# Kernel optimization log

Hardware: AMD Instinct MI355X
Metric: run time of the kernel (lower is better)

## Reference

```python
import jax, jax.numpy as jnp
import numpy as np

NUM_HEADS = 12
LN_EPS = 1e-5


def _layernorm(x, w, b):
    m = jnp.mean(x, axis=-1, keepdims=True)
    v = jnp.mean(jnp.square(x - m), axis=-1, keepdims=True)
    return (x - m) * jax.lax.rsqrt(v + LN_EPS) * w + b


def setup_inputs() -> dict:
    key = jax.random.key(0)
    ks = jax.random.split(key, 6)
    B, N, C, H = 8, 1024, 768, 3072
    s = 0.02
    return {
        "x": jax.random.normal(ks[0], (B, N, C), jnp.float32),
        "ln1_w": jnp.ones((C,), jnp.float32),
        "ln1_b": jnp.zeros((C,), jnp.float32),
        "qkv_w": jax.random.normal(ks[1], (3 * C, C), jnp.float32) * s,
        "qkv_b": jnp.zeros((3 * C,), jnp.float32),
        "proj_w": jax.random.normal(ks[2], (C, C), jnp.float32) * s,
        "proj_b": jnp.zeros((C,), jnp.float32),
        "ln2_w": jnp.ones((C,), jnp.float32),
        "ln2_b": jnp.zeros((C,), jnp.float32),
        "fc1_w": jax.random.normal(ks[3], (H, C), jnp.float32) * s,
        "fc1_b": jnp.zeros((H,), jnp.float32),
        "fc2_w": jax.random.normal(ks[4], (C, H), jnp.float32) * s,
        "fc2_b": jnp.zeros((C,), jnp.float32),
    }


def reference(x, ln1_w, ln1_b, qkv_w, qkv_b, proj_w, proj_b,
              ln2_w, ln2_b, fc1_w, fc1_b, fc2_w, fc2_b):
    B, N, C = x.shape
    H = NUM_HEADS
    d = C // H
    scale = d ** (-0.5)

    # --- attention on norm1(x) (size=None path, dropout rates are 0) ---
    h = _layernorm(x, ln1_w, ln1_b)
    qkv = h @ qkv_w.T + qkv_b                      # [B,N,3C]
    qkv = qkv.reshape(B, N, 3, H, d).transpose(2, 0, 3, 1, 4)  # [3,B,H,N,d]
    q, k, v = qkv[0], qkv[1], qkv[2]
    attn = jnp.einsum('bhqd,bhkd->bhqk', q, k) * scale
    attn = jax.nn.softmax(attn, axis=-1)
    o = jnp.einsum('bhqk,bhkd->bhqd', attn, v)     # [B,H,N,d]
    o = o.transpose(0, 2, 1, 3).reshape(B, N, C)
    x_attn = o @ proj_w.T + proj_b

    # --- residual + MLP ---
    x = x + x_attn
    h2 = _layernorm(x, ln2_w, ln2_b)
    h2 = jax.nn.gelu(h2 @ fc1_w.T + fc1_b, approximate=False)
    x = x + (h2 @ fc2_w.T + fc2_b)
    return x
```

## Files before the change

### kernel.cpp

```cpp
#include <hip/hip_runtime.h>
#include <cmath>

typedef __bf16 bf16;
typedef __bf16 bf16x8 __attribute__((ext_vector_type(8)));
typedef __bf16 bf16x4 __attribute__((ext_vector_type(4)));
typedef float floatx4 __attribute__((ext_vector_type(4)));

#define MFMA16(A, B, C) __builtin_amdgcn_mfma_f32_16x16x32_bf16((A), (B), (C), 0, 0, 0)

#define GLDS16(g, l)                                                   \
  __builtin_amdgcn_global_load_lds(                                    \
      (const __attribute__((address_space(1))) void*)(g),              \
      (__attribute__((address_space(3))) void*)(l), 16, 0, 0)

__global__ __launch_bounds__(256) void pre_kernel(
    const float* __restrict__ x, const float* __restrict__ g,
    const float* __restrict__ be, bf16* __restrict__ h1,
    const float* __restrict__ s0, bf16* __restrict__ d0, int n0,
    const float* __restrict__ s1, bf16* __restrict__ d1, int n1,
    const float* __restrict__ s2, bf16* __restrict__ d2, int n2,
    const float* __restrict__ s3, bf16* __restrict__ d3, int n3) {
  int bid = blockIdx.x;
  int t = threadIdx.x;
  if (bid < 8192) {
    const float* xr = x + (size_t)bid * 768;
    float v0 = xr[t], v1 = xr[t + 256], v2 = xr[t + 512];
    float s = v0 + v1 + v2;
    float s2 = v0 * v0 + v1 * v1 + v2 * v2;
#pragma unroll
    for (int o = 1; o < 64; o <<= 1) {
      s += __shfl_xor(s, o, 64);
      s2 += __shfl_xor(s2, o, 64);
    }
    __shared__ float red[8];
    int w = t >> 6, lane = t & 63;
    if (lane == 0) { red[w] = s; red[4 + w] = s2; }
    __syncthreads();
    float ts = red[0] + red[1] + red[2] + red[3];
    float ts2 = red[4] + red[5] + red[6] + red[7];
    float mean = ts * (1.0f / 768.0f);
    float var = ts2 * (1.0f / 768.0f) - mean * mean;
    float rstd = rsqrtf(var + 1e-5f);
    bf16* orow = h1 + (size_t)bid * 768;
    orow[t]       = (bf16)((v0 - mean) * rstd * g[t]       + be[t]);
    orow[t + 256] = (bf16)((v1 - mean) * rstd * g[t + 256] + be[t + 256]);
    orow[t + 512] = (bf16)((v2 - mean) * rstd * g[t + 512] + be[t + 512]);
    return;
  }
  int i = (bid - 8192) * 256 + t;
  const float* s;
  bf16* d;
  if (i < n0) { s = s0 + (size_t)i * 4; d = d0 + (size_t)i * 4; }
  else if ((i -= n0) < n1) { s = s1 + (size_t)i * 4; d = d1 + (size_t)i * 4; }
  else if ((i -= n1) < n2) { s = s2 + (size_t)i * 4; d = d2 + (size_t)i * 4; }
  else if ((i -= n2) < n3) { s = s3 + (size_t)i * 4; d = d3 + (size_t)i * 4; }
  else return;
  bf16x4 v;
  v[0] = (bf16)s[0]; v[1] = (bf16)s[1]; v[2] = (bf16)s[2]; v[3] = (bf16)s[3];
  *(bf16x4*)d = v;
}

__global__ __launch_bounds__(256) void ln_kernel(const float* __restrict__ x,
                                                 const float* __restrict__ g,
                                                 const float* __restrict__ be,
                                                 bf16* __restrict__ out) {
  int row = blockIdx.x;
  int t = threadIdx.x;
  const float* xr = x + (size_t)row * 768;
  float v0 = xr[t], v1 = xr[t + 256], v2 = xr[t + 512];
  float s = v0 + v1 + v2;
  float s2 = v0 * v0 + v1 * v1 + v2 * v2;
#pragma unroll
  for (int o = 1; o < 64; o <<= 1) {
    s += __shfl_xor(s, o, 64);
    s2 += __shfl_xor(s2, o, 64);
  }
  __shared__ float red[8];
  int w = t >> 6, lane = t & 63;
  if (lane == 0) { red[w] = s; red[4 + w] = s2; }
  __syncthreads();
  float ts = red[0] + red[1] + red[2] + red[3];
  float ts2 = red[4] + red[5] + red[6] + red[7];
  float mean = ts * (1.0f / 768.0f);
  float var = ts2 * (1.0f / 768.0f) - mean * mean;
  float rstd = rsqrtf(var + 1e-5f);
  bf16* orow = out + (size_t)row * 768;
  orow[t]       = (bf16)((v0 - mean) * rstd * g[t]       + be[t]);
  orow[t + 256] = (bf16)((v1 - mean) * rstd * g[t + 256] + be[t + 256]);
  orow[t + 512] = (bf16)((v2 - mean) * rstd * g[t + 512] + be[t + 512]);
}

constexpr int EP_BF16 = 0;
constexpr int EP_RES_F32 = 1;
constexpr int EP_GELU_BF16 = 2;

template <int EP, int NJ>
__global__ __launch_bounds__(256, 3) void gemm_bt(
    const bf16* __restrict__ A, const bf16* __restrict__ Bw,
    const float* __restrict__ bias, const float* __restrict__ resid,
    void* __restrict__ outp, int M, int N, int K) {
  __shared__ alignas(16) bf16 Asl[128 * 64];
  __shared__ alignas(16) bf16 Bsl[NJ * 32 * 64];
  int tid = threadIdx.x;
  int lane = tid & 63, w = tid >> 6;
  int wm = w >> 1, wn = w & 1;
  int q16 = lane & 15, quad = lane >> 4;
  int fid = blockIdx.x + gridDim.x * blockIdx.y;
  int nb = gridDim.x;
  int s = fid >> 3;
  int m0 = ((fid & 7) * (gridDim.y >> 3) + s / nb) * 128;
  int n0 = (s % nb) * (NJ * 32);

  floatx4 acc[4][NJ];
#pragma unroll
  for (int i = 0; i < 4; i++)
#pragma unroll
    for (int j = 0; j < NJ; j++) acc[i][j] = (floatx4){0.f, 0.f, 0.f, 0.f};

  int rIn = lane >> 3;
  int cg = (lane & 7) ^ rIn;
  const bf16* ag[4];
  const bf16* bg[NJ];
#pragma unroll
  for (int q = 0; q < 4; q++)
    ag[q] = A + (size_t)(m0 + (w * 4 + q) * 8 + rIn) * K + cg * 8;
#pragma unroll
  for (int q = 0; q < NJ; q++)
    bg[q] = Bw + (size_t)(n0 + (w * NJ + q) * 8 + rIn) * K + cg * 8;
  bf16* la = &Asl[w * 2048];
  bf16* lb = &Bsl[w * NJ * 512];

  int msel = q16 & 7;
  int offA[2][4], offB[2][NJ];
#pragma unroll
  for (int ks = 0; ks < 2; ks++) {
#pragma unroll
    for (int i = 0; i < 4; i++)
      offA[ks][i] = (wm * 64 + i * 16 + q16) * 64 + (((ks * 4 + quad) ^ msel)) * 8;
#pragma unroll
    for (int j = 0; j < NJ; j++)
      offB[ks][j] = (wn * 16 * NJ + j * 16 + q16) * 64 + (((ks * 4 + quad) ^ msel)) * 8;
  }

  for (int k0 = 0; k0 < K; k0 += 64) {
    __syncthreads();
#pragma unroll
    for (int q = 0; q < 4; q++) {
      GLDS16(ag[q], la + q * 512);
      ag[q] += 64;
    }
#pragma unroll
    for (int q = 0; q < NJ; q++) {
      GLDS16(bg[q], lb + q * 512);
      bg[q] += 64;
    }
    __syncthreads();
#pragma unroll
    for (int ks = 0; ks < 2; ks++) {
      bf16x8 af[4], bfr[NJ];
#pragma unroll
      for (int i = 0; i < 4; i++) af[i] = *(const bf16x8*)&Asl[offA[ks][i]];
#pragma unroll
      for (int j = 0; j < NJ; j++) bfr[j] = *(const bf16x8*)&Bsl[offB[ks][j]];
#pragma unroll
      for (int i = 0; i < 4; i++)
#pragma unroll
        for (int j = 0; j < NJ; j++) acc[i][j] = MFMA16(af[i], bfr[j], acc[i][j]);
    }
  }

#pragma unroll
  for (int i = 0; i < 4; i++) {
#pragma unroll
    for (int j = 0; j < NJ; j++) {
#pragma unroll
      for (int r = 0; r < 4; r++) {
        int m = m0 + wm * 64 + i * 16 + quad * 4 + r;
        int n = n0 + wn * 16 * NJ + j * 16 + q16;
        size_t idx = (size_t)m * N + n;
        float v = acc[i][j][r] + bias[n];
        if constexpr (EP == EP_BF16) {
          ((bf16*)outp)[idx] = (bf16)v;
        } else if constexpr (EP == EP_RES_F32) {
          ((float*)outp)[idx] = v + resid[idx];
        } else {
          float u = v * (2.3022083f + 0.1029443f * v * v);
          float e = __builtin_amdgcn_exp2f(-u);
          float gv = v * __builtin_amdgcn_rcpf(1.0f + e);
          ((bf16*)outp)[idx] = (bf16)gv;
        }
      }
    }
  }
}

__global__ __launch_bounds__(256) void vt_kernel(const bf16* __restrict__ qkv,
                                                 bf16* __restrict__ VT) {
  __shared__ bf16 T[64 * 74];
  int t = threadIdx.x;
  int bh = blockIdx.y;
  int b = bh / 12, h = bh % 12;
  int kt = blockIdx.x;
  int kloc = t >> 2;
  int d0 = (t & 3) * 16;
  const bf16* src = qkv + (size_t)(b * 1024 + kt * 64 + kloc) * 2304 + 1536 +
                    h * 64 + d0;
  bf16x8 a = *(const bf16x8*)src;
  bf16x8 c = *(const bf16x8*)(src + 8);
#pragma unroll
  for (int e = 0; e < 8; e++) T[(d0 + e) * 74 + kloc] = a[e];
#pragma unroll
  for (int e = 0; e < 8; e++) T[(d0 + 8 + e) * 74 + kloc] = c[e];
  __syncthreads();
  int d = t >> 2;
  int k0 = (t & 3) * 16;
  bf16x8 r0, r1;
#pragma unroll
  for (int e = 0; e < 8; e++) r0[e] = T[d * 74 + k0 + e];
#pragma unroll
  for (int e = 0; e < 8; e++) r1[e] = T[d * 74 + k0 + 8 + e];
  bf16* dst = VT + ((size_t)bh * 64 + d) * 1024 + kt * 64 + k0;
  *(bf16x8*)dst = r0;
  *(bf16x8*)(dst + 8) = r1;
}

__global__ __launch_bounds__(256, 4) void attn_kernel(const bf16* __restrict__ qkv,
                                                      const bf16* __restrict__ VT,
                                                      bf16* __restrict__ o) {
  __shared__ alignas(16) bf16 Pl[4][2][16 * 40];
  int tid = threadIdx.x;
  int lane = tid & 63, w = tid >> 6;
  int q16 = lane & 15, quad = lane >> 4;
  int bh = blockIdx.y;
  int b = bh / 12, h = bh % 12;
  int qbase = blockIdx.x * 128 + w * 32;
  const int KS = 32 * 2304;

  bf16x8 qf[2][2];
#pragma unroll
  for (int qt = 0; qt < 2; qt++)
#pragma unroll
    for (int c = 0; c < 2; c++)
      qf[qt][c] = *(const bf16x8*)(qkv +
          (size_t)(b * 1024 + qbase + qt * 16 + q16) * 2304 + h * 64 +
          c * 32 + quad * 8);

  const bf16* kp[2];
#pragma unroll
  for (int nc = 0; nc < 2; nc++)
    kp[nc] = qkv + (size_t)(b * 1024 + nc * 16 + q16) * 2304 + 768 + h * 64 +
             quad * 8;
  const bf16* vp[4];
#pragma unroll
  for (int dc = 0; dc < 4; dc++)
    vp[dc] = VT + ((size_t)bh * 64 + dc * 16 + q16) * 1024 + quad * 8;

  const bf16* pread = &Pl[w][0][q16 * 40 + quad * 8];
  int pw_base = (quad * 4) * 40 + q16;

  float l_[2][4];
  floatx4 oacc[2][4];
#pragma unroll
  for (int qt = 0; qt < 2; qt++)
#pragma unroll
    for (int r = 0; r < 4; r++) l_[qt][r] = 0.f;
#pragma unroll
  for (int qt = 0; qt < 2; qt++)
#pragma unroll
    for (int dc = 0; dc < 4; dc++) oacc[qt][dc] = (floatx4){0.f, 0.f, 0.f, 0.f};

  for (int kt = 0; kt < 32; kt++) {
    bf16x8 kf[2][2];
#pragma unroll
    for (int nc = 0; nc < 2; nc++) {
#pragma unroll
      for (int ck = 0; ck < 2; ck++)
        kf[nc][ck] = *(const bf16x8*)(kp[nc] + ck * 32);
      kp[nc] += KS;
    }
    bf16x8 vf[4];
#pragma unroll
    for (int dc = 0; dc < 4; dc++) {
      vf[dc] = *(const bf16x8*)vp[dc];
      vp[dc] += 32;
    }

#pragma unroll
    for (int qt = 0; qt < 2; qt++) {
#pragma unroll
      for (int nc = 0; nc < 2; nc++) {
        floatx4 z = (floatx4){0.f, 0.f, 0.f, 0.f};
        z = MFMA16(qf[qt][0], kf[nc][0], z);
        z = MFMA16(qf[qt][1], kf[nc][1], z);
#pragma unroll
        for (int r = 0; r < 4; r++) {
          float p = __builtin_amdgcn_exp2f(z[r] * 0.18033688011f);
          l_[qt][r] += p;
          Pl[w][qt][pw_base + r * 40 + nc * 16] = (bf16)p;
        }
      }
    }

#pragma unroll
    for (int qt = 0; qt < 2; qt++) {
      bf16x8 pf = *(const bf16x8*)(pread + qt * 640);
#pragma unroll
      for (int dc = 0; dc < 4; dc++)
        oacc[qt][dc] = MFMA16(pf, vf[dc], oacc[qt][dc]);
    }
  }

#pragma unroll
  for (int qt = 0; qt < 2; qt++) {
    bf16* op = o + (size_t)(b * 1024 + qbase + qt * 16) * 768 + h * 64;
#pragma unroll
    for (int r = 0; r < 4; r++) {
      float s = l_[qt][r];
#pragma unroll
      for (int off = 1; off < 16; off <<= 1) s += __shfl_xor(s, off, 16);
      float inv = 1.0f / s;
#pragma unroll
      for (int dc = 0; dc < 4; dc++)
        op[(size_t)(quad * 4 + r) * 768 + dc * 16 + q16] =
            (bf16)(oacc[qt][dc][r] * inv);
    }
  }
}

extern "C" void kernel_launch(void* const* d_in, const int* in_sizes, int n_in,
                              void* d_out, int out_size, void* d_ws, size_t ws_size,
                              hipStream_t stream) {
  (void)in_sizes; (void)n_in; (void)out_size; (void)ws_size;
  const float* x      = (const float*)d_in[0];
  const float* ln1_w  = (const float*)d_in[1];
  const float* ln1_b  = (const float*)d_in[2];
  const float* qkv_w  = (const float*)d_in[3];
  const float* qkv_b  = (const float*)d_in[4];
  const float* proj_w = (const float*)d_in[5];
  const float* proj_b = (const float*)d_in[6];
  const float* ln2_w  = (const float*)d_in[7];
  const float* ln2_b  = (const float*)d_in[8];
  const float* fc1_w  = (const float*)d_in[9];
  const float* fc1_b  = (const float*)d_in[10];
  const float* fc2_w  = (const float*)d_in[11];
  const float* fc2_b  = (const float*)d_in[12];

  char* ws = (char*)d_ws;
  size_t off = 0;
  auto alloc = [&](size_t bytes) {
    void* p = ws + off;
    off += (bytes + 255) & ~(size_t)255;
    return p;
  };
  bf16* wq  = (bf16*)alloc((size_t)2304 * 768 * 2);
  bf16* wp  = (bf16*)alloc((size_t)768 * 768 * 2);
  bf16* wf1 = (bf16*)alloc((size_t)3072 * 768 * 2);
  bf16* wf2 = (bf16*)alloc((size_t)768 * 3072 * 2);
  bf16* slotA = (bf16*)alloc((size_t)8192 * 768 * 2);
  bf16* slotB = (bf16*)alloc((size_t)8192 * 3072 * 2);
  float* x1 = (float*)alloc((size_t)8192 * 768 * 4);
  bf16* VT = (bf16*)alloc((size_t)96 * 64 * 1024 * 2);

  bf16* h1 = slotA;
  bf16* qkvb = slotB;
  bf16* ob = slotA;
  bf16* h2 = slotA;
  bf16* hm = slotB;

  pre_kernel<<<8192 + 6912, 256, 0, stream>>>(
      x, ln1_w, ln1_b, h1,
      qkv_w, wq, 2304 * 768 / 4, proj_w, wp, 768 * 768 / 4,
      fc1_w, wf1, 3072 * 768 / 4, fc2_w, wf2, 768 * 3072 / 4);

  gemm_bt<EP_BF16, 4><<<dim3(18, 64), 256, 0, stream>>>(
      h1, wq, qkv_b, nullptr, qkvb, 8192, 2304, 768);
  vt_kernel<<<dim3(16, 96), 256, 0, stream>>>(qkvb, VT);
  attn_kernel<<<dim3(8, 96), 256, 0, stream>>>(qkvb, VT, ob);
  gemm_bt<EP_RES_F32, 2><<<dim3(12, 64), 256, 0, stream>>>(
      ob, wp, proj_b, x, x1, 8192, 768, 768);
  ln_kernel<<<8192, 256, 0, stream>>>(x1, ln2_w, ln2_b, h2);
  gemm_bt<EP_GELU_BF16, 4><<<dim3(24, 64), 256, 0, stream>>>(
      h2, wf1, fc1_b, nullptr, hm, 8192, 3072, 768);
  gemm_bt<EP_RES_F32, 2><<<dim3(12, 64), 256, 0, stream>>>(
      hm, wf2, fc2_b, x1, (float*)d_out, 8192, 768, 3072);
}
```

Baseline: 367.0 us.

## Stage K/V tiles in LDS with async double buffering and transpose S

The attention kernel now loads each 32-key K and V tile once per block into swizzled LDS through global_load_lds, double buffered so the next tile's load overlaps the current tile's compute. It no longer has every wave read K and V straight from global memory. S is computed transposed (K as the A operand), so the softmax probabilities land directly in registers in the layout the 16x16x16 MFMA needs. This removes the per-tile LDS round trip for P. Block indexing is flattened so that consecutive blocks map to different batches, which changes L2 locality. The cost is a block-wide barrier every iteration and twice as many smaller MFMAs for P·V.

```diff
diff --git a/kernel.cpp b/kernel.cpp
--- a/kernel.cpp
+++ b/kernel.cpp
@@ -5,8 +5,14 @@
 typedef __bf16 bf16x8 __attribute__((ext_vector_type(8)));
 typedef __bf16 bf16x4 __attribute__((ext_vector_type(4)));
 typedef float floatx4 __attribute__((ext_vector_type(4)));
+typedef short short4v __attribute__((ext_vector_type(4)));
 
 #define MFMA16(A, B, C) __builtin_amdgcn_mfma_f32_16x16x32_bf16((A), (B), (C), 0, 0, 0)
+
+static __device__ __forceinline__ floatx4 mfma_k16(bf16x4 a, bf16x4 b, floatx4 c) {
+  return __builtin_amdgcn_mfma_f32_16x16x16bf16_1k(
+      __builtin_bit_cast(short4v, a), __builtin_bit_cast(short4v, b), c, 0, 0, 0);
+}
 
 #define GLDS16(g, l)                                                   \
   __builtin_amdgcn_global_load_lds(                                    \
@@ -227,13 +233,15 @@
 __global__ __launch_bounds__(256, 4) void attn_kernel(const bf16* __restrict__ qkv,
                                                       const bf16* __restrict__ VT,
                                                       bf16* __restrict__ o) {
-  __shared__ alignas(16) bf16 Pl[4][2][16 * 40];
+  __shared__ alignas(16) bf16 Kl[2][32 * 64];
+  __shared__ alignas(16) bf16 Vl[2][64 * 32];
   int tid = threadIdx.x;
   int lane = tid & 63, w = tid >> 6;
   int q16 = lane & 15, quad = lane >> 4;
-  int bh = blockIdx.y;
-  int b = bh / 12, h = bh % 12;
-  int qbase = blockIdx.x * 128 + w * 32;
+  int f = blockIdx.x;
+  int b = f & 7, idx = f >> 3;
+  int h = idx % 12;
+  int qbase = (idx / 12) * 128 + w * 32;
   const int KS = 32 * 2304;
 
   bf16x8 qf[2][2];
@@ -245,84 +253,103 @@
           (size_t)(b * 1024 + qbase + qt * 16 + q16) * 2304 + h * 64 +
           c * 32 + quad * 8);
 
-  const bf16* kp[2];
+  int kkey = w * 8 + (lane >> 3);
+  int kchunk = (lane & 7) ^ (lane >> 3);
+  const bf16* kg = qkv + (size_t)(b * 1024 + kkey) * 2304 + 768 + h * 64 +
+                   kchunk * 8;
+  bf16* kd[2] = {&Kl[0][w * 512], &Kl[1][w * 512]};
+
+  const bf16* vg = VT + ((size_t)(b * 12 + h) * 64 + w * 16 + (lane >> 2)) * 1024 +
+                   (lane & 3) * 8;
+  bf16* vd[2] = {&Vl[0][w * 512], &Vl[1][w * 512]};
+
+  int koff[2][2];
 #pragma unroll
   for (int nc = 0; nc < 2; nc++)
-    kp[nc] = qkv + (size_t)(b * 1024 + nc * 16 + q16) * 2304 + 768 + h * 64 +
-             quad * 8;
-  const bf16* vp[4];
+#pragma unroll
+    for (int ck = 0; ck < 2; ck++) {
+      int key = nc * 16 + q16;
+      koff[nc][ck] = (key * 8 + ((ck * 4 + quad) ^ (key & 7))) * 8;
+    }
+  int voff[4][2];
 #pragma unroll
   for (int dc = 0; dc < 4; dc++)
-    vp[dc] = VT + ((size_t)bh * 64 + dc * 16 + q16) * 1024 + quad * 8;
-
-  const bf16* pread = &Pl[w][0][q16 * 40 + quad * 8];
-  int pw_base = (quad * 4) * 40 + q16;
-
-  float l_[2][4];
+#pragma unroll
+    for (int nc = 0; nc < 2; nc++)
+      voff[dc][nc] = (dc * 64 + q16 * 4 + nc * 2 + (quad >> 1)) * 8 + (quad & 1) * 4;
+
+  float l_[2] = {0.f, 0.f};
   floatx4 oacc[2][4];
 #pragma unroll
   for (int qt = 0; qt < 2; qt++)
 #pragma unroll
-    for (int r = 0; r < 4; r++) l_[qt][r] = 0.f;
-#pragma unroll
-  for (int qt = 0; qt < 2; qt++)
-#pragma unroll
     for (int dc = 0; dc < 4; dc++) oacc[qt][dc] = (floatx4){0.f, 0.f, 0.f, 0.f};
 
+  GLDS16(kg, kd[0]);
+  kg += KS;
+  GLDS16(vg, vd[0]);
+  vg += 32;
+
   for (int kt = 0; kt < 32; kt++) {
+    int cur = kt & 1, nxt = cur ^ 1;
+    __syncthreads();
+    if (kt < 31) {
+      GLDS16(kg, kd[nxt]);
+      kg += KS;
+      GLDS16(vg, vd[nxt]);
+      vg += 32;
+    }
+
     bf16x8 kf[2][2];
 #pragma unroll
-    for (int nc = 0; nc < 2; nc++) {
+    for (int nc = 0; nc < 2; nc++)
 #pragma unroll
       for (int ck = 0; ck < 2; ck++)
-        kf[nc][ck] = *(const bf16x8*)(kp[nc] + ck * 32);
-      kp[nc] += KS;
-    }
-    bf16x8 vf[4];
-#pragma unroll
-    for (int dc = 0; dc < 4; dc++) {
-      vf[dc] = *(const bf16x8*)vp[dc];
-      vp[dc] += 32;
-    }
+        kf[nc][ck] = *(const bf16x8*)&Kl[cur][koff[nc][ck]];
+    bf16x4 vf[4][2];
+#pragma unroll
+    for (int dc = 0; dc < 4; dc++)
+#pragma unroll
+      for (int nc = 0; nc < 2; nc++)
+        vf[dc][nc] = *(const bf16x4*)&Vl[cur][voff[dc][nc]];
 
 #pragma unroll
     for (int qt = 0; qt < 2; qt++) {
 #pragma unroll
       for (int nc = 0; nc < 2; nc++) {
         floatx4 z = (floatx4){0.f, 0.f, 0.f, 0.f};
-        z = MFMA16(qf[qt][0], kf[nc][0], z);
-        z = MFMA16(qf[qt][1], kf[nc][1], z);
+        z = MFMA16(kf[nc][0], qf[qt][0], z);
+        z = MFMA16(kf[nc][1], qf[qt][1], z);
+        bf16x4 pfrag;
+        float psum = 0.f;
 #pragma unroll
         for (int r = 0; r < 4; r++) {
           float p = __builtin_amdgcn_exp2f(z[r] * 0.18033688011f);
-          l_[qt][r] += p;
-          Pl[w][qt][pw_base + r * 40 + nc * 16] = (bf16)p;
+          psum += p;
+          pfrag[r] = (bf16)p;
         }
+        l_[qt] += psum;
+#pragma unroll
+        for (int dc = 0; dc < 4; dc++)
+          oacc[qt][dc] = mfma_k16(vf[dc][nc], pfrag, oacc[qt][dc]);
       }
     }
-
-#pragma unroll
-    for (int qt = 0; qt < 2; qt++) {
-      bf16x8 pf = *(const bf16x8*)(pread + qt * 640);
-#pragma unroll
-      for (int dc = 0; dc < 4; dc++)
-        oacc[qt][dc] = MFMA16(pf, vf[dc], oacc[qt][dc]);
-    }
   }
 
 #pragma unroll
   for (int qt = 0; qt < 2; qt++) {
-    bf16* op = o + (size_t)(b * 1024 + qbase + qt * 16) * 768 + h * 64;
-#pragma unroll
-    for (int r = 0; r < 4; r++) {
-      float s = l_[qt][r];
-#pragma unroll
-      for (int off = 1; off < 16; off <<= 1) s += __shfl_xor(s, off, 16);
-      float inv = 1.0f / s;
-#pragma unroll
-      for (int dc = 0; dc < 4; dc++)
-        op[(size_t)(quad * 4 + r) * 768 + dc * 16 + q16] =
-            (bf16)(oacc[qt][dc][r] * inv);
+    float s = l_[qt];
+    s += __shfl_xor(s, 16, 64);
+    s += __shfl_xor(s, 32, 64);
+    float inv = 1.0f / s;
+    bf16* op = o + (size_t)(b * 1024 + qbase + qt * 16 + q16) * 768 + h * 64 +
+               quad * 4;
+#pragma unroll
+    for (int dc = 0; dc < 4; dc++) {
+      bf16x4 ov;
+#pragma unroll
+      for (int r = 0; r < 4; r++) ov[r] = (bf16)(oacc[qt][dc][r] * inv);
+      *(bf16x4*)(op + dc * 16) = ov;
     }
   }
 }
@@ -375,7 +402,7 @@
   gemm_bt<EP_BF16, 4><<<dim3(18, 64), 256, 0, stream>>>(
       h1, wq, qkv_b, nullptr, qkvb, 8192, 2304, 768);
   vt_kernel<<<dim3(16, 96), 256, 0, stream>>>(qkvb, VT);
-  attn_kernel<<<dim3(8, 96), 256, 0, stream>>>(qkvb, VT, ob);
+  attn_kernel<<<768, 256, 0, stream>>>(qkvb, VT, ob);
   gemm_bt<EP_RES_F32, 2><<<dim3(12, 64), 256, 0, stream>>>(
       ob, wp, proj_b, x, x1, 8192, 768, 768);
   ln_kernel<<<8192, 256, 0, stream>>>(x1, ln2_w, ln2_b, h2);
```

Result: faster. 340.7 us (-7.2%).
